# Optimization experiments

Hardware: AMD Instinct MI355X
Metric: run time of the kernel (lower is better)

## Reference

```python
import jax, jax.numpy as jnp
import numpy as np

# D2Q9 lattice velocities (standard ordering: rest, axis, diagonal)
E = np.array([[0,0],[1,0],[0,1],[-1,0],[0,-1],[1,1],[-1,1],[-1,-1],[1,-1]], dtype=np.int64)

# Gram-Schmidt moment matrix, row order matches the layer's eq stack:
# [rho, jx, jy, e, eps, qx, qy, pxx, pxy]
_M_np = np.array([
    [ 1,  1,  1,  1,  1,  1,  1,  1,  1],  # rho
    [ 0,  1,  0, -1,  0,  1, -1, -1,  1],  # jx
    [ 0,  0,  1,  0, -1,  1,  1, -1, -1],  # jy
    [-4, -1, -1, -1, -1,  2,  2,  2,  2],  # e
    [ 4, -2, -2, -2, -2,  1,  1,  1,  1],  # eps
    [ 0, -2,  0,  2,  0,  1, -1, -1,  1],  # qx
    [ 0,  0, -2,  0,  2,  1,  1, -1, -1],  # qy
    [ 0,  1, -1,  1, -1,  0,  0,  0,  0],  # pxx
    [ 0,  0,  0,  0,  0,  1, -1,  1, -1],  # pxy
], dtype=np.float64)
_Minv_np = np.linalg.inv(_M_np)

TAU = 0.6
GX, GY = 0.0, -1e-4
ITERATIONS = 4
NX, NY = 1024, 1024


def _stream(f):
    # periodic streaming: shift each population along its lattice velocity
    return jnp.stack(
        [jnp.roll(f[..., i], (int(E[i, 0]), int(E[i, 1])), axis=(0, 1)) for i in range(9)],
        axis=-1,
    )


def setup_inputs() -> dict:
    key = jax.random.key(0)
    kf, kw = jax.random.split(key)
    f = jax.random.uniform(kf, (NX, NY, 9), dtype=jnp.float32)
    w = jax.random.normal(kw, (7,), dtype=jnp.float32)
    return {"f": f, "w": w}


def reference(f, w):
    M = jnp.asarray(_M_np, dtype=f.dtype)
    Minv = jnp.asarray(_Minv_np, dtype=f.dtype)
    ex = jnp.asarray(E[:, 0], dtype=f.dtype)
    ey = jnp.asarray(E[:, 1], dtype=f.dtype)
    inv_tau = jnp.asarray(1.0 / TAU, dtype=f.dtype)

    for _ in range(ITERATIONS):
        # handle_boundaries: periodic (no solid nodes) -> no-op
        f = _stream(f)
        # macroscopic fields
        rho = jnp.sum(f, axis=-1)                      # [X,Y]
        vx = jnp.einsum("xyq,q->xy", f, ex) / rho
        vy = jnp.einsum("xyq,q->xy", f, ey) / rho
        # equilibrium moments with learned coefficients (gravity forcing via tau shift)
        ux = vx + TAU * GX * rho
        uy = vy + TAU * GY * rho
        jx = rho * ux
        jy = rho * uy
        j2 = jx * jx + jy * jy
        e_m = w[0] * rho + w[1] * j2
        eps = w[2] * rho - w[3] * j2
        qx = w[4] * jx
        qy = w[4] * jy
        pxx = w[5] * (jx * jx - jy * jy)
        pxy = w[6] * jx * jy
        meq = jnp.stack([rho, jx, jy, e_m, eps, qx, qy, pxx, pxy], axis=2)
        # collision in moment space, single relaxation rate 1/tau
        m = jnp.einsum("xyq,pq->xyp", f, M)
        m = m - inv_tau * (m - meq)
        f = jnp.einsum("xyp,qp->xyq", m, Minv)
    return f
```

## Files before the change

kernel.cpp:

```cpp
#include <hip/hip_runtime.h>


#define NXD 1024
#define NYD 1024
#define NCELL (NXD * NYD)
#define ROWF (NYD * 9)

constexpr float INV_TAU = (float)(1.0 / 0.6);
constexpr float TGY     = (float)(0.6 * -1e-4);

__device__ __forceinline__ void collide1(
    float f0, float f1, float f2, float f3, float f4,
    float f5, float f6, float f7, float f8,
    const float (&w)[7],
    float& o0, float& o1, float& o2, float& o3, float& o4,
    float& o5, float& o6, float& o7, float& o8)
{
    const float rho = f0 + f1 + f2 + f3 + f4 + f5 + f6 + f7 + f8;
    const float jx0 = f1 - f3 + f5 - f6 - f7 + f8;
    const float jy0 = f2 - f4 + f5 + f6 - f7 - f8;
    const float vx = jx0 / rho;
    const float vy = jy0 / rho;
    const float uy = vy + TGY * rho;
    const float jx = rho * vx;
    const float jy = rho * uy;
    const float j2 = jx * jx + jy * jy;

    const float ax = f1 + f2 + f3 + f4;
    const float dg = f5 + f6 + f7 + f8;
    const float m3 = -4.f * f0 - ax + 2.f * dg;
    const float m4 =  4.f * f0 - 2.f * ax + dg;
    const float m5 = -2.f * f1 + 2.f * f3 + f5 - f6 - f7 + f8;
    const float m6 = -2.f * f2 + 2.f * f4 + f5 + f6 - f7 - f8;
    const float m7 = f1 - f2 + f3 - f4;
    const float m8 = f5 - f6 + f7 - f8;

    const float me3 = w[0] * rho + w[1] * j2;
    const float me4 = w[2] * rho - w[3] * j2;
    const float me5 = w[4] * jx;
    const float me6 = w[4] * jy;
    const float me7 = w[5] * (jx * jx - jy * jy);
    const float me8 = w[6] * (jx * jy);

    const float mp1 = jx0 - INV_TAU * (jx0 - jx);
    const float mp2 = jy0 - INV_TAU * (jy0 - jy);
    const float mp3 = m3  - INV_TAU * (m3 - me3);
    const float mp4 = m4  - INV_TAU * (m4 - me4);
    const float mp5 = m5  - INV_TAU * (m5 - me5);
    const float mp6 = m6  - INV_TAU * (m6 - me6);
    const float mp7 = m7  - INV_TAU * (m7 - me7);
    const float mp8 = m8  - INV_TAU * (m8 - me8);

    const float s0 = rho * (1.f / 9.f);
    const float s1 = mp1 * (1.f / 6.f);
    const float s2 = mp2 * (1.f / 6.f);
    const float s3 = mp3 * (1.f / 36.f);
    const float s4 = mp4 * (1.f / 36.f);
    const float s5 = mp5 * (1.f / 12.f);
    const float s6 = mp6 * (1.f / 12.f);
    const float s7 = mp7 * 0.25f;
    const float s8 = mp8 * 0.25f;

    const float h0 = s0 - s3 - 2.f * s4;
    const float g0 = s0 + 2.f * s3 + s4;

    o0 = s0 - 4.f * s3 + 4.f * s4;
    o1 = h0 + s1 - 2.f * s5 + s7;
    o2 = h0 + s2 - 2.f * s6 - s7;
    o3 = h0 - s1 + 2.f * s5 + s7;
    o4 = h0 - s2 + 2.f * s6 - s7;
    o5 = g0 + s1 + s2 + s5 + s6 + s8;
    o6 = g0 - s1 + s2 - s5 + s6 - s8;
    o7 = g0 - s1 - s2 - s5 - s6 + s8;
    o8 = g0 + s1 - s2 + s5 - s6 - s8;
}

__device__ __forceinline__ void collide4(const float4 (&F)[9], float4 (&O)[9],
                                         const float (&w)[7]) {
    #pragma unroll
    for (int j = 0; j < 4; ++j) {
        float f[9], o[9];
        #pragma unroll
        for (int q = 0; q < 9; ++q)
            f[q] = ((const float*)&F[q])[j];
        collide1(f[0], f[1], f[2], f[3], f[4], f[5], f[6], f[7], f[8], w,
                 o[0], o[1], o[2], o[3], o[4], o[5], o[6], o[7], o[8]);
        #pragma unroll
        for (int q = 0; q < 9; ++q)
            ((float*)&O[q])[j] = o[q];
    }
}

__device__ __forceinline__ void load_w(const float* __restrict__ wp,
                                       float (&w)[7]) {
    #pragma unroll
    for (int i = 0; i < 7; ++i) w[i] = wp[i];
}

__device__ __forceinline__ void push_store(float* __restrict__ dst,
                                           const float4 (&P)[9],
                                           float (&E)[256][7],
                                           int x, int t) {
    const int y0 = t << 2;
    E[t][0] = P[2].w;  E[t][1] = P[5].w;  E[t][2] = P[6].w;
    E[t][3] = P[4].x;  E[t][4] = P[7].x;  E[t][5] = P[8].x;
    __syncthreads();
    const int tm = (t - 1) & 255, tp = (t + 1) & 255;
    const float4 S2 = make_float4(E[tm][0], P[2].x, P[2].y, P[2].z);
    const float4 S5 = make_float4(E[tm][1], P[5].x, P[5].y, P[5].z);
    const float4 S6 = make_float4(E[tm][2], P[6].x, P[6].y, P[6].z);
    const float4 S4 = make_float4(P[4].y, P[4].z, P[4].w, E[tp][3]);
    const float4 S7 = make_float4(P[7].y, P[7].z, P[7].w, E[tp][4]);
    const float4 S8 = make_float4(P[8].y, P[8].z, P[8].w, E[tp][5]);
    const int xp = (x + 1) & (NXD - 1), xm = (x - 1) & (NXD - 1);
    *(float4*)(dst + 0 * NCELL + x  * NYD + y0) = P[0];
    *(float4*)(dst + 1 * NCELL + xp * NYD + y0) = P[1];
    *(float4*)(dst + 3 * NCELL + xm * NYD + y0) = P[3];
    *(float4*)(dst + 2 * NCELL + x  * NYD + y0) = S2;
    *(float4*)(dst + 5 * NCELL + xp * NYD + y0) = S5;
    *(float4*)(dst + 6 * NCELL + xm * NYD + y0) = S6;
    *(float4*)(dst + 4 * NCELL + x  * NYD + y0) = S4;
    *(float4*)(dst + 7 * NCELL + xm * NYD + y0) = S7;
    *(float4*)(dst + 8 * NCELL + xp * NYD + y0) = S8;
}

__global__ __launch_bounds__(256) void k1_push(const float* __restrict__ src,
                                               float* __restrict__ dst) {
    __shared__ float E[256][7];
    const int x = blockIdx.x, t = threadIdx.x;

    float4 A[9];
    const float* base = src + (size_t)x * ROWF + t * 36;
    #pragma unroll
    for (int q = 0; q < 9; ++q)
        A[q] = *(const float4*)(base + 4 * q);

    const float* a = (const float*)A;
    float4 P[9];
    #pragma unroll
    for (int q = 0; q < 9; ++q)
        P[q] = make_float4(a[q], a[9 + q], a[18 + q], a[27 + q]);

    push_store(dst, P, E, x, t);
}

__global__ __launch_bounds__(256) void k_cs(const float* __restrict__ src,
                                            float* __restrict__ dst,
                                            const float* __restrict__ wp) {
    __shared__ float E[256][7];
    const int x = blockIdx.x, t = threadIdx.x;
    const int y0 = t << 2;

    float4 F[9];
    #pragma unroll
    for (int q = 0; q < 9; ++q)
        F[q] = *(const float4*)(src + q * NCELL + x * NYD + y0);

    float w[7];
    load_w(wp, w);

    float4 O[9];
    collide4(F, O, w);

    push_store(dst, O, E, x, t);
}

__global__ __launch_bounds__(256) void k5_aos(const float* __restrict__ src,
                                              float* __restrict__ dst,
                                              const float* __restrict__ wp) {
    __shared__ float4 T[ROWF / 4];
    const int x = blockIdx.x, t = threadIdx.x;
    const int y0 = t << 2;

    float4 F[9];
    #pragma unroll
    for (int q = 0; q < 9; ++q)
        F[q] = *(const float4*)(src + q * NCELL + x * NYD + y0);

    float w[7];
    load_w(wp, w);

    float4 O[9];
    collide4(F, O, w);

    float* tt = (float*)(T + t * 9);
    #pragma unroll
    for (int j = 0; j < 4; ++j) {
        #pragma unroll
        for (int q = 0; q < 9; ++q)
            tt[j * 9 + q] = ((const float*)&O[q])[j];
    }
    __syncthreads();

    float4* dv = (float4*)(dst + (size_t)x * ROWF);
    #pragma unroll
    for (int it = 0; it < 9; ++it)
        dv[t + it * 256] = T[t + it * 256];
}

__global__ __launch_bounds__(256) void lbm_step_aos(const float* __restrict__ src,
                                                    float* __restrict__ dst,
                                                    const float* __restrict__ wp) {
    const int cell = blockIdx.x * 256 + threadIdx.x;
    const int x = cell >> 10;
    const int y = cell & (NYD - 1);
    const int xm = (x + NXD - 1) & (NXD - 1);
    const int xp = (x + 1) & (NXD - 1);
    const int ym = (y + NYD - 1) & (NYD - 1);
    const int yp = (y + 1) & (NYD - 1);

    const float f0 = src[(x  * NYD + y ) * 9 + 0];
    const float f1 = src[(xm * NYD + y ) * 9 + 1];
    const float f2 = src[(x  * NYD + ym) * 9 + 2];
    const float f3 = src[(xp * NYD + y ) * 9 + 3];
    const float f4 = src[(x  * NYD + yp) * 9 + 4];
    const float f5 = src[(xm * NYD + ym) * 9 + 5];
    const float f6 = src[(xp * NYD + ym) * 9 + 6];
    const float f7 = src[(xp * NYD + yp) * 9 + 7];
    const float f8 = src[(xm * NYD + yp) * 9 + 8];

    float w[7];
    load_w(wp, w);
    float o0,o1,o2,o3,o4,o5,o6,o7,o8;
    collide1(f0,f1,f2,f3,f4,f5,f6,f7,f8, w,
             o0,o1,o2,o3,o4,o5,o6,o7,o8);

    float* o = dst + (size_t)(x * NYD + y) * 9;
    o[0]=o0; o[1]=o1; o[2]=o2; o[3]=o3; o[4]=o4; o[5]=o5; o[6]=o6; o[7]=o7; o[8]=o8;
}

extern "C" void kernel_launch(void* const* d_in, const int* in_sizes, int n_in,
                              void* d_out, int out_size, void* d_ws, size_t ws_size,
                              hipStream_t stream) {
    const float* f_in = (const float*)d_in[0];
    const float* w    = (const float*)d_in[1];
    float* out = (float*)d_out;
    float* A   = (float*)d_ws;
    const size_t bufBytes = (size_t)NCELL * 9 * sizeof(float);

    dim3 grid(NXD), block(256);

    if (ws_size >= 2 * bufBytes) {
        float* B = A + (size_t)NCELL * 9;
        k1_push<<<grid, block, 0, stream>>>(f_in, A);
        k_cs   <<<grid, block, 0, stream>>>(A, B, w);
        k_cs   <<<grid, block, 0, stream>>>(B, A, w);
        k_cs   <<<grid, block, 0, stream>>>(A, B, w);
        k5_aos <<<grid, block, 0, stream>>>(B, out, w);
    } else {
        float* fin_mut = (float*)d_in[0];
        lbm_step_aos<<<4096, 256, 0, stream>>>(f_in, out, w);
        lbm_step_aos<<<4096, 256, 0, stream>>>(out, fin_mut, w);
        lbm_step_aos<<<4096, 256, 0, stream>>>(fin_mut, out, w);
        lbm_step_aos<<<4096, 256, 0, stream>>>(out, fin_mut, w);
        hipMemcpyAsync(d_out, fin_mut, bufBytes, hipMemcpyDeviceToDevice, stream);
    }
}
```

Baseline: 135.9 us.

## Switch LBM pipeline from push-streaming to pull-streaming with half-row blocks

Moves streaming from the store side (push) to the load side (pull). Each step now reads neighbor rows and gets the y-halo values through wavefront shuffles, with a direct global load at wave edges, so the shared-memory exchange and __syncthreads are gone. Blocks shrink to 128 threads covering half a row, which doubles the grid. The initial transpose now goes through an LDS staging buffer so that global reads are coalesced. The trade-off is more scattered, partially redundant edge loads and loads from neighboring x rows.

```diff
diff --git a/kernel.cpp b/kernel.cpp
--- a/kernel.cpp
+++ b/kernel.cpp
@@ -5,6 +5,8 @@
 #define NYD 1024
 #define NCELL (NXD * NYD)
 #define ROWF (NYD * 9)
+#define HALF (NYD / 2)
+#define HROWF (HALF * 9)
 
 constexpr float INV_TAU = (float)(1.0 / 0.6);
 constexpr float TGY     = (float)(0.6 * -1e-4);
@@ -97,64 +99,92 @@
     for (int i = 0; i < 7; ++i) w[i] = wp[i];
 }
 
-__device__ __forceinline__ void push_store(float* __restrict__ dst,
-                                           const float4 (&P)[9],
-                                           float (&E)[256][7],
-                                           int x, int t) {
-    const int y0 = t << 2;
-    E[t][0] = P[2].w;  E[t][1] = P[5].w;  E[t][2] = P[6].w;
-    E[t][3] = P[4].x;  E[t][4] = P[7].x;  E[t][5] = P[8].x;
+__device__ __forceinline__ float edge_up(const float4 own,
+                                         const float* __restrict__ rowp,
+                                         int y0, int t) {
+    float e = __shfl_up(own.w, 1, 64);
+    if ((t & 63) == 0) e = rowp[(y0 - 1) & (NYD - 1)];
+    return e;
+}
+__device__ __forceinline__ float edge_dn(const float4 own,
+                                         const float* __restrict__ rowp,
+                                         int y0, int t) {
+    float e = __shfl_down(own.x, 1, 64);
+    if ((t & 63) == 63) e = rowp[(y0 + 4) & (NYD - 1)];
+    return e;
+}
+
+__device__ __forceinline__ void pull9(const float* __restrict__ src,
+                                      int x, int y0, int t, float4 (&F)[9]) {
+    const int xm = (x - 1) & (NXD - 1), xp = (x + 1) & (NXD - 1);
+    const float* p0 = src + 0 * NCELL + x  * NYD;
+    const float* p1 = src + 1 * NCELL + xm * NYD;
+    const float* p2 = src + 2 * NCELL + x  * NYD;
+    const float* p3 = src + 3 * NCELL + xp * NYD;
+    const float* p4 = src + 4 * NCELL + x  * NYD;
+    const float* p5 = src + 5 * NCELL + xm * NYD;
+    const float* p6 = src + 6 * NCELL + xp * NYD;
+    const float* p7 = src + 7 * NCELL + xp * NYD;
+    const float* p8 = src + 8 * NCELL + xm * NYD;
+
+    F[0] = *(const float4*)(p0 + y0);
+    F[1] = *(const float4*)(p1 + y0);
+    F[3] = *(const float4*)(p3 + y0);
+    const float4 o2 = *(const float4*)(p2 + y0);
+    const float4 o5 = *(const float4*)(p5 + y0);
+    const float4 o6 = *(const float4*)(p6 + y0);
+    const float4 o4 = *(const float4*)(p4 + y0);
+    const float4 o7 = *(const float4*)(p7 + y0);
+    const float4 o8 = *(const float4*)(p8 + y0);
+
+    const float e2 = edge_up(o2, p2, y0, t);
+    const float e5 = edge_up(o5, p5, y0, t);
+    const float e6 = edge_up(o6, p6, y0, t);
+    const float e4 = edge_dn(o4, p4, y0, t);
+    const float e7 = edge_dn(o7, p7, y0, t);
+    const float e8 = edge_dn(o8, p8, y0, t);
+
+    F[2] = make_float4(e2, o2.x, o2.y, o2.z);
+    F[5] = make_float4(e5, o5.x, o5.y, o5.z);
+    F[6] = make_float4(e6, o6.x, o6.y, o6.z);
+    F[4] = make_float4(o4.y, o4.z, o4.w, e4);
+    F[7] = make_float4(o7.y, o7.z, o7.w, e7);
+    F[8] = make_float4(o8.y, o8.z, o8.w, e8);
+}
+
+__global__ __launch_bounds__(128) void k0_t(const float* __restrict__ src,
+                                            float* __restrict__ dst) {
+    __shared__ float4 T[HROWF / 4];
+    const int b = blockIdx.x, t = threadIdx.x;
+    const int x = b >> 1, h = b & 1;
+
+    const float4* s = (const float4*)(src + (size_t)x * ROWF + h * HROWF);
+    #pragma unroll
+    for (int i = 0; i < 9; ++i)
+        T[t + 128 * i] = s[t + 128 * i];
     __syncthreads();
-    const int tm = (t - 1) & 255, tp = (t + 1) & 255;
-    const float4 S2 = make_float4(E[tm][0], P[2].x, P[2].y, P[2].z);
-    const float4 S5 = make_float4(E[tm][1], P[5].x, P[5].y, P[5].z);
-    const float4 S6 = make_float4(E[tm][2], P[6].x, P[6].y, P[6].z);
-    const float4 S4 = make_float4(P[4].y, P[4].z, P[4].w, E[tp][3]);
-    const float4 S7 = make_float4(P[7].y, P[7].z, P[7].w, E[tp][4]);
-    const float4 S8 = make_float4(P[8].y, P[8].z, P[8].w, E[tp][5]);
-    const int xp = (x + 1) & (NXD - 1), xm = (x - 1) & (NXD - 1);
-    *(float4*)(dst + 0 * NCELL + x  * NYD + y0) = P[0];
-    *(float4*)(dst + 1 * NCELL + xp * NYD + y0) = P[1];
-    *(float4*)(dst + 3 * NCELL + xm * NYD + y0) = P[3];
-    *(float4*)(dst + 2 * NCELL + x  * NYD + y0) = S2;
-    *(float4*)(dst + 5 * NCELL + xp * NYD + y0) = S5;
-    *(float4*)(dst + 6 * NCELL + xm * NYD + y0) = S6;
-    *(float4*)(dst + 4 * NCELL + x  * NYD + y0) = S4;
-    *(float4*)(dst + 7 * NCELL + xm * NYD + y0) = S7;
-    *(float4*)(dst + 8 * NCELL + xp * NYD + y0) = S8;
-}
-
-__global__ __launch_bounds__(256) void k1_push(const float* __restrict__ src,
-                                               float* __restrict__ dst) {
-    __shared__ float E[256][7];
-    const int x = blockIdx.x, t = threadIdx.x;
 
     float4 A[9];
-    const float* base = src + (size_t)x * ROWF + t * 36;
+    #pragma unroll
+    for (int k = 0; k < 9; ++k) A[k] = T[t * 9 + k];
+    const float* a = (const float*)A;
+
+    const int c = x * NYD + h * HALF + 4 * t;
     #pragma unroll
     for (int q = 0; q < 9; ++q)
-        A[q] = *(const float4*)(base + 4 * q);
-
-    const float* a = (const float*)A;
-    float4 P[9];
-    #pragma unroll
-    for (int q = 0; q < 9; ++q)
-        P[q] = make_float4(a[q], a[9 + q], a[18 + q], a[27 + q]);
-
-    push_store(dst, P, E, x, t);
-}
-
-__global__ __launch_bounds__(256) void k_cs(const float* __restrict__ src,
+        *(float4*)(dst + q * NCELL + c) =
+            make_float4(a[q], a[9 + q], a[18 + q], a[27 + q]);
+}
+
+__global__ __launch_bounds__(128) void k_sc(const float* __restrict__ src,
                                             float* __restrict__ dst,
                                             const float* __restrict__ wp) {
-    __shared__ float E[256][7];
-    const int x = blockIdx.x, t = threadIdx.x;
-    const int y0 = t << 2;
+    const int b = blockIdx.x, t = threadIdx.x;
+    const int x  = b >> 1;
+    const int y0 = (b & 1) * HALF + 4 * t;
 
     float4 F[9];
-    #pragma unroll
-    for (int q = 0; q < 9; ++q)
-        F[q] = *(const float4*)(src + q * NCELL + x * NYD + y0);
+    pull9(src, x, y0, t, F);
 
     float w[7];
     load_w(wp, w);
@@ -162,20 +192,22 @@
     float4 O[9];
     collide4(F, O, w);
 
-    push_store(dst, O, E, x, t);
-}
-
-__global__ __launch_bounds__(256) void k5_aos(const float* __restrict__ src,
+    const int c = x * NYD + y0;
+    #pragma unroll
+    for (int q = 0; q < 9; ++q)
+        *(float4*)(dst + q * NCELL + c) = O[q];
+}
+
+__global__ __launch_bounds__(128) void k4_aos(const float* __restrict__ src,
                                               float* __restrict__ dst,
                                               const float* __restrict__ wp) {
-    __shared__ float4 T[ROWF / 4];
-    const int x = blockIdx.x, t = threadIdx.x;
-    const int y0 = t << 2;
+    __shared__ float4 T[HROWF / 4];
+    const int b = blockIdx.x, t = threadIdx.x;
+    const int x  = b >> 1;
+    const int y0 = (b & 1) * HALF + 4 * t;
 
     float4 F[9];
-    #pragma unroll
-    for (int q = 0; q < 9; ++q)
-        F[q] = *(const float4*)(src + q * NCELL + x * NYD + y0);
+    pull9(src, x, y0, t, F);
 
     float w[7];
     load_w(wp, w);
@@ -183,19 +215,16 @@
     float4 O[9];
     collide4(F, O, w);
 
-    float* tt = (float*)(T + t * 9);
-    #pragma unroll
-    for (int j = 0; j < 4; ++j) {
-        #pragma unroll
-        for (int q = 0; q < 9; ++q)
-            tt[j * 9 + q] = ((const float*)&O[q])[j];
-    }
+    float* tt = (float*)&T[t * 9];
+    #pragma unroll
+    for (int f = 0; f < 36; ++f)
+        tt[f] = ((const float*)&O[f % 9])[f / 9];
     __syncthreads();
 
-    float4* dv = (float4*)(dst + (size_t)x * ROWF);
-    #pragma unroll
-    for (int it = 0; it < 9; ++it)
-        dv[t + it * 256] = T[t + it * 256];
+    float4* dv = (float4*)(dst + (size_t)x * ROWF + (b & 1) * HROWF);
+    #pragma unroll
+    for (int i = 0; i < 9; ++i)
+        dv[t + 128 * i] = T[t + 128 * i];
 }
 
 __global__ __launch_bounds__(256) void lbm_step_aos(const float* __restrict__ src,
@@ -238,15 +267,15 @@
     float* A   = (float*)d_ws;
     const size_t bufBytes = (size_t)NCELL * 9 * sizeof(float);
 
-    dim3 grid(NXD), block(256);
+    dim3 grid(NXD * 2), block(128);
 
     if (ws_size >= 2 * bufBytes) {
         float* B = A + (size_t)NCELL * 9;
-        k1_push<<<grid, block, 0, stream>>>(f_in, A);
-        k_cs   <<<grid, block, 0, stream>>>(A, B, w);
-        k_cs   <<<grid, block, 0, stream>>>(B, A, w);
-        k_cs   <<<grid, block, 0, stream>>>(A, B, w);
-        k5_aos <<<grid, block, 0, stream>>>(B, out, w);
+        k0_t  <<<grid, block, 0, stream>>>(f_in, A);
+        k_sc  <<<grid, block, 0, stream>>>(A, B, w);
+        k_sc  <<<grid, block, 0, stream>>>(B, A, w);
+        k_sc  <<<grid, block, 0, stream>>>(A, B, w);
+        k4_aos<<<grid, block, 0, stream>>>(B, out, w);
     } else {
         float* fin_mut = (float*)d_in[0];
         lbm_step_aos<<<4096, 256, 0, stream>>>(f_in, out, w);
```

Result: slower. 143.4 us (+5.5%).
